# Optimization experiments

Hardware: AMD Instinct MI355X
Metric: run time of the kernel (lower is better)

The kernel has to match this reference:

```python
import jax, jax.numpy as jnp
import numpy as np

N_NODES = 100000
N_EDGES = 1250000
D_FEAT = 64
DROPOUT_PROB = 0.7  # graph edge dropout; keep_prob = 1 - DROPOUT_PROB


def setup_inputs() -> dict:
    key = jax.random.key(0)
    k1, k2, k3, k4 = jax.random.split(key, 4)
    feature = jax.random.normal(k1, (N_NODES, D_FEAT), dtype=jnp.float32)
    edge_w = jax.random.uniform(k2, (N_EDGES,), dtype=jnp.float32)
    src = jax.random.randint(k3, (N_EDGES,), 0, N_NODES, dtype=jnp.int32)
    dst = jax.random.randint(k4, (N_EDGES,), 0, N_NODES, dtype=jnp.int32)
    return {"feature": feature, "edge_w": edge_w, "src": src, "dst": dst}


def reference(feature, edge_w, src, dst):
    N, d = feature.shape
    E = edge_w.shape[0]

    # --- graph_dropout: mask int((1-keep_prob)*E) random edge indices (with replacement) to 0 ---
    drop_size = int(DROPOUT_PROB * E)
    ridx = jax.random.randint(jax.random.fold_in(jax.random.key(0), 1),
                              (drop_size,), 0, E, dtype=jnp.int32)
    w = edge_w.at[ridx].set(0.0)

    # --- structural degree norms (DGL GraphConv norm='both', clamp(min=1)) ---
    ones_e = jnp.ones((E,), dtype=feature.dtype)
    out_deg = jax.ops.segment_sum(ones_e, src, num_segments=N)
    in_deg = jax.ops.segment_sum(ones_e, dst, num_segments=N)
    norm_out = jnp.maximum(out_deg, 1.0) ** -0.5  # [N]
    norm_in = jnp.maximum(in_deg, 1.0) ** -0.5    # [N]

    def graph_conv(h):
        h = h * norm_out[:, None]                 # pre-normalize by src degree
        msg = h[src] * w[:, None]                 # [E, d] edge-weighted messages
        h = jax.ops.segment_sum(msg, dst, num_segments=N)
        return h * norm_in[:, None]               # post-normalize by dst degree

    h = feature
    embs = [feature]
    for _ in range(2):
        h = graph_conv(h)
        embs.append(h)  # F.dropout in original is a no-op (result discarded)

    return jnp.mean(jnp.stack(embs, axis=1), axis=1)  # [N, d]
```

## Files before the change

### kernel.cpp

```cpp
#include <hip/hip_runtime.h>
#include <stdint.h>

#define N_NODES 100000
#define N_EDGES 1250000
#define D_FEAT 64
#define DROP_SIZE 875000
#define CAP 64

struct TF { uint32_t a, b; };

__host__ __device__ constexpr TF tf2x32(uint32_t k0, uint32_t k1, uint32_t x0, uint32_t x1) {
  uint32_t ks[3] = {k0, k1, k0 ^ k1 ^ 0x1BD11BDAu};
  const int rot[8] = {13, 15, 26, 6, 17, 29, 16, 24};
  x0 += ks[0]; x1 += ks[1];
  for (int g = 0; g < 5; ++g) {
    for (int j = 0; j < 4; ++j) {
      int r = rot[(g & 1) * 4 + j];
      x0 += x1;
      x1 = (x1 << r) | (x1 >> (32 - r));
      x1 ^= x0;
    }
    x0 += ks[(g + 1) % 3];
    x1 += ks[(g + 2) % 3] + (uint32_t)(g + 1);
  }
  return TF{x0, x1};
}

constexpr TF KEYA = tf2x32(0u, 0u, 0u, 1u);
constexpr TF K2   = tf2x32(KEYA.a, KEYA.b, 0u, 1u);

#define OFF_DROPPED 0u
#define OFF_PACKED  1250048u
#define OFF_DEGOUT  1650048u
#define ZERO_BYTES  2050048u
#define OFF_NOUT    2050048u
#define OFF_NIN     2450048u
#define OFF_PAIRS   2850048u
#define OFF_H1      54050048u
#define WS_NEEDED   79650048u

__global__ __launch_bounds__(256) void k_drop(unsigned char* dropped) {
  int i = blockIdx.x * 256 + threadIdx.x;
  if (i >= DROP_SIZE) return;
  TF r = tf2x32(K2.a, K2.b, 0u, (uint32_t)i);
  uint32_t bits = r.a ^ r.b;
  dropped[bits % (uint32_t)N_EDGES] = 1;
}

__global__ __launch_bounds__(256) void k_build(const int* __restrict__ src,
                                               const int* __restrict__ dst,
                                               const float* __restrict__ ew,
                                               const unsigned char* __restrict__ dropped,
                                               int* deg_out, unsigned* packed,
                                               int2* __restrict__ pairs) {
  int e = blockIdx.x * 256 + threadIdx.x;
  if (e >= N_EDGES) return;
  int s = src[e], d = dst[e];
  atomicAdd(&deg_out[s], 1);
  float w = ew[e];
  bool kept = (!dropped[e]) && (w != 0.0f);
  unsigned add = 1u + (kept ? (1u << 16) : 0u);
  unsigned old = atomicAdd(&packed[d], add);
  if (kept) {
    unsigned slot = old >> 16;
    pairs[(unsigned)d * CAP + slot] = make_int2(s, __float_as_int(w));
  }
}

__global__ __launch_bounds__(256) void k_norm(const unsigned* __restrict__ packed,
                                              const int* __restrict__ deg_out,
                                              float* nout, float* nin) {
  int n = blockIdx.x * 256 + threadIdx.x;
  if (n >= N_NODES) return;
  int din = (int)(packed[n] & 0xFFFFu);
  int dou = deg_out[n];
  nin[n]  = 1.0f / sqrtf((float)(din > 1 ? din : 1));
  nout[n] = 1.0f / sqrtf((float)(dou > 1 ? dou : 1));
}

template <bool FINAL>
__global__ __launch_bounds__(256) void k_conv(const int2* __restrict__ pairs,
                                              const unsigned* __restrict__ packed,
                                              const float* __restrict__ nin,
                                              const float* __restrict__ nout,
                                              const float* __restrict__ gin,
                                              const float* __restrict__ feat,
                                              float* __restrict__ out0) {
  int w = (blockIdx.x * blockDim.x + threadIdx.x) >> 6;
  int lane = threadIdx.x & 63;
  if (w >= N_NODES) return;
  int c = (int)(packed[w] >> 16);
  int2 pr = make_int2(0, 0);
  float ns = 0.0f;
  if (lane < c) {
    pr = pairs[(unsigned)w * CAP + lane];
    ns = nout[pr.x];
  }
  float coef = __int_as_float(pr.y) * ns;
  float nw = nin[w];
  float acc = 0.0f;
  int c4 = (c + 3) & ~3;
  for (int k = 0; k < c4; k += 4) {
    int   s0 = __shfl(pr.x, k);     float f0 = __shfl(coef, k);
    int   s1 = __shfl(pr.x, k + 1); float f1 = __shfl(coef, k + 1);
    int   s2 = __shfl(pr.x, k + 2); float f2 = __shfl(coef, k + 2);
    int   s3 = __shfl(pr.x, k + 3); float f3 = __shfl(coef, k + 3);
    float g0 = gin[s0 * D_FEAT + lane];
    float g1 = gin[s1 * D_FEAT + lane];
    float g2 = gin[s2 * D_FEAT + lane];
    float g3 = gin[s3 * D_FEAT + lane];
    acc = fmaf(f0, g0, acc);
    acc = fmaf(f1, g1, acc);
    acc = fmaf(f2, g2, acc);
    acc = fmaf(f3, g3, acc);
  }
  float h = acc * nw;
  int idx = w * D_FEAT + lane;
  if (FINAL) {
    out0[idx] = (feat[idx] + gin[idx] + h) / 3.0f;
  } else {
    out0[idx] = h;
  }
}

extern "C" void kernel_launch(void* const* d_in, const int* in_sizes, int n_in,
                              void* d_out, int out_size, void* d_ws, size_t ws_size,
                              hipStream_t stream) {
  if (ws_size < (size_t)WS_NEEDED) return;

  const float* feature = (const float*)d_in[0];
  const float* edge_w  = (const float*)d_in[1];
  const int*   src     = (const int*)d_in[2];
  const int*   dst     = (const int*)d_in[3];
  float* out = (float*)d_out;

  char* ws = (char*)d_ws;
  unsigned char* dropped = (unsigned char*)(ws + OFF_DROPPED);
  unsigned* packed = (unsigned*)(ws + OFF_PACKED);
  int*      deg_out = (int*)(ws + OFF_DEGOUT);
  float*    nout = (float*)(ws + OFF_NOUT);
  float*    nin  = (float*)(ws + OFF_NIN);
  int2*     pairs = (int2*)(ws + OFF_PAIRS);
  float*    h1   = (float*)(ws + OFF_H1);

  hipMemsetAsync(ws, 0, ZERO_BYTES, stream);

  k_drop<<<(DROP_SIZE + 255) / 256, 256, 0, stream>>>(dropped);
  k_build<<<(N_EDGES + 255) / 256, 256, 0, stream>>>(src, dst, edge_w, dropped,
                                                     deg_out, packed, pairs);
  k_norm<<<(N_NODES + 255) / 256, 256, 0, stream>>>(packed, deg_out, nout, nin);
  k_conv<false><<<(N_NODES * D_FEAT + 255) / 256, 256, 0, stream>>>(
      pairs, packed, nin, nout, feature, nullptr, h1);
  k_conv<true><<<(N_NODES * D_FEAT + 255) / 256, 256, 0, stream>>>(
      pairs, packed, nin, nout, h1, feature, out);
}
```

Measured before the change: 279.8 us.

## Privatize degree and slot atomics per XCD and compact adjacency afterwards

The edge-build kernel now reads the hardware XCD id and gives each XCD its own copy of the degree and slot counters. It uses workgroup-scope relaxed atomics on these copies and writes each edge into a per-XCD region of 8 slots per destination node. Extra edges go to a small overflow list capped at 4 per node. A new compaction kernel, one wave per node, merges the per-XCD regions and overflow entries with ballot and popcount, sums the degrees and computes the norms. The goal is to cut cross-die atomic contention, at the cost of an extra pass and more workspace. It relies on workgroup-scope atomics staying coherent within one XCD's L2, and on the overflow caps never being exceeded.

```diff
diff --git a/kernel.cpp b/kernel.cpp
--- a/kernel.cpp
+++ b/kernel.cpp
@@ -5,7 +5,8 @@
 #define N_EDGES 1250000
 #define D_FEAT 64
 #define DROP_SIZE 875000
-#define CAP 64
+#define NXCD 8
+#define RCAP 8
 
 struct TF { uint32_t a, b; };
 
@@ -30,14 +31,17 @@
 constexpr TF K2   = tf2x32(KEYA.a, KEYA.b, 0u, 1u);
 
 #define OFF_DROPPED 0u
-#define OFF_PACKED  1250048u
-#define OFF_DEGOUT  1650048u
-#define ZERO_BYTES  2050048u
-#define OFF_NOUT    2050048u
-#define OFF_NIN     2450048u
-#define OFF_PAIRS   2850048u
-#define OFF_H1      54050048u
-#define WS_NEEDED   79650048u
+#define OFF_PACKEDX 1250048u
+#define OFF_DEGOUTX 4450048u
+#define OFF_OVCNT   7650048u
+#define ZERO_BYTES  8050048u
+#define OFF_NOUT    8050048u
+#define OFF_NIN     8450048u
+#define OFF_CNT     8850048u
+#define OFF_OV      9250048u
+#define OFF_PAIRS   12450048u
+#define OFF_H1      63650048u
+#define WS_NEEDED   89250048u
 
 __global__ __launch_bounds__(256) void k_drop(unsigned char* dropped) {
   int i = blockIdx.x * 256 + threadIdx.x;
@@ -51,36 +55,72 @@
                                                const int* __restrict__ dst,
                                                const float* __restrict__ ew,
                                                const unsigned char* __restrict__ dropped,
-                                               int* deg_out, unsigned* packed,
+                                               int* degoutx, unsigned* packedx,
+                                               unsigned* ovcnt, int2* __restrict__ ov,
                                                int2* __restrict__ pairs) {
   int e = blockIdx.x * 256 + threadIdx.x;
   if (e >= N_EDGES) return;
+  unsigned xcd = (unsigned)__builtin_amdgcn_s_getreg(63508) & (NXCD - 1);
   int s = src[e], d = dst[e];
-  atomicAdd(&deg_out[s], 1);
+  __hip_atomic_fetch_add(&degoutx[xcd * N_NODES + s], 1,
+                         __ATOMIC_RELAXED, __HIP_MEMORY_SCOPE_WORKGROUP);
   float w = ew[e];
   bool kept = (!dropped[e]) && (w != 0.0f);
   unsigned add = 1u + (kept ? (1u << 16) : 0u);
-  unsigned old = atomicAdd(&packed[d], add);
+  unsigned old = __hip_atomic_fetch_add(&packedx[xcd * N_NODES + d], add,
+                                        __ATOMIC_RELAXED, __HIP_MEMORY_SCOPE_WORKGROUP);
   if (kept) {
     unsigned slot = old >> 16;
-    pairs[(unsigned)d * CAP + slot] = make_int2(s, __float_as_int(w));
-  }
-}
-
-__global__ __launch_bounds__(256) void k_norm(const unsigned* __restrict__ packed,
-                                              const int* __restrict__ deg_out,
-                                              float* nout, float* nin) {
-  int n = blockIdx.x * 256 + threadIdx.x;
+    int2 entry = make_int2(s, __float_as_int(w));
+    if (slot < RCAP) {
+      pairs[(unsigned)d * 64 + xcd * RCAP + slot] = entry;
+    } else {
+      unsigned os = atomicAdd(&ovcnt[d], 1u);
+      if (os < 4) ov[(unsigned)d * 4 + os] = entry;
+    }
+  }
+}
+
+__global__ __launch_bounds__(256) void k_compact(const unsigned* __restrict__ packedx,
+                                                 const int* __restrict__ degoutx,
+                                                 const unsigned* __restrict__ ovcnt,
+                                                 const int2* __restrict__ ov,
+                                                 int2* __restrict__ pairs,
+                                                 unsigned* __restrict__ cnt,
+                                                 float* nout, float* nin) {
+  int n = (blockIdx.x * 256 + threadIdx.x) >> 6;
+  int lane = threadIdx.x & 63;
   if (n >= N_NODES) return;
-  int din = (int)(packed[n] & 0xFFFFu);
-  int dou = deg_out[n];
-  nin[n]  = 1.0f / sqrtf((float)(din > 1 ? din : 1));
-  nout[n] = 1.0f / sqrtf((float)(dou > 1 ? dou : 1));
+  int region = lane >> 3, slot = lane & 7;
+  unsigned pk = packedx[region * N_NODES + n];
+  int dox = degoutx[region * N_NODES + n];
+  int cr = (int)(pk >> 16); if (cr > RCAP) cr = RCAP;
+  bool valid = slot < cr;
+  int2 entry = make_int2(0, 0);
+  if (valid) entry = pairs[(unsigned)n * 64 + lane];
+  int din = (slot == 0) ? (int)(pk & 0xFFFFu) : 0;
+  int dou = (slot == 0) ? dox : 0;
+  #pragma unroll
+  for (int off = 32; off; off >>= 1) {
+    din += __shfl_xor(din, off);
+    dou += __shfl_xor(dou, off);
+  }
+  unsigned long long mask = __ballot(valid);
+  int rank = __popcll(mask & ((1ull << lane) - 1ull));
+  int total = __popcll(mask);
+  if (valid) pairs[(unsigned)n * 64 + rank] = entry;
+  int ovn = (int)ovcnt[n]; if (ovn > 4) ovn = 4;
+  if (lane == 0) {
+    for (int j = 0; j < ovn; ++j) pairs[(unsigned)n * 64 + total + j] = ov[(unsigned)n * 4 + j];
+    cnt[n] = (unsigned)(total + ovn);
+    nin[n]  = 1.0f / sqrtf((float)(din > 1 ? din : 1));
+    nout[n] = 1.0f / sqrtf((float)(dou > 1 ? dou : 1));
+  }
 }
 
 template <bool FINAL>
 __global__ __launch_bounds__(256) void k_conv(const int2* __restrict__ pairs,
-                                              const unsigned* __restrict__ packed,
+                                              const unsigned* __restrict__ cnt,
                                               const float* __restrict__ nin,
                                               const float* __restrict__ nout,
                                               const float* __restrict__ gin,
@@ -89,11 +129,11 @@
   int w = (blockIdx.x * blockDim.x + threadIdx.x) >> 6;
   int lane = threadIdx.x & 63;
   if (w >= N_NODES) return;
-  int c = (int)(packed[w] >> 16);
+  int c = (int)cnt[w];
   int2 pr = make_int2(0, 0);
   float ns = 0.0f;
   if (lane < c) {
-    pr = pairs[(unsigned)w * CAP + lane];
+    pr = pairs[(unsigned)w * 64 + lane];
     ns = nout[pr.x];
   }
   float coef = __int_as_float(pr.y) * ns;
@@ -136,10 +176,13 @@
 
   char* ws = (char*)d_ws;
   unsigned char* dropped = (unsigned char*)(ws + OFF_DROPPED);
-  unsigned* packed = (unsigned*)(ws + OFF_PACKED);
-  int*      deg_out = (int*)(ws + OFF_DEGOUT);
+  unsigned* packedx = (unsigned*)(ws + OFF_PACKEDX);
+  int*      degoutx = (int*)(ws + OFF_DEGOUTX);
+  unsigned* ovcnt   = (unsigned*)(ws + OFF_OVCNT);
   float*    nout = (float*)(ws + OFF_NOUT);
   float*    nin  = (float*)(ws + OFF_NIN);
+  unsigned* cnt  = (unsigned*)(ws + OFF_CNT);
+  int2*     ov   = (int2*)(ws + OFF_OV);
   int2*     pairs = (int2*)(ws + OFF_PAIRS);
   float*    h1   = (float*)(ws + OFF_H1);
 
@@ -147,10 +190,11 @@
 
   k_drop<<<(DROP_SIZE + 255) / 256, 256, 0, stream>>>(dropped);
   k_build<<<(N_EDGES + 255) / 256, 256, 0, stream>>>(src, dst, edge_w, dropped,
-                                                     deg_out, packed, pairs);
-  k_norm<<<(N_NODES + 255) / 256, 256, 0, stream>>>(packed, deg_out, nout, nin);
+                                                     degoutx, packedx, ovcnt, ov, pairs);
+  k_compact<<<(N_NODES * 64 + 255) / 256, 256, 0, stream>>>(packedx, degoutx, ovcnt, ov,
+                                                            pairs, cnt, nout, nin);
   k_conv<false><<<(N_NODES * D_FEAT + 255) / 256, 256, 0, stream>>>(
-      pairs, packed, nin, nout, feature, nullptr, h1);
+      pairs, cnt, nin, nout, feature, nullptr, h1);
   k_conv<true><<<(N_NODES * D_FEAT + 255) / 256, 256, 0, stream>>>(
-      pairs, packed, nin, nout, h1, feature, out);
-}
+      pairs, cnt, nin, nout, h1, feature, out);
+}
```

New measurement: 310.4 us. 1.11x slower.
